# Optimization experiments

Measured on AMD Instinct MI355X. Metric: run time of the kernel, lower is better.

The kernel has to match this reference:

```python
import jax, jax.numpy as jnp
import numpy as np

N = 40000   # nodes
E = 500000  # edges
H = 2       # attention heads
C = 128     # d_graph_layer (in==out per layer)
L = 3       # n_graph_layer
G = 800     # graphs in batch
FIN = 56    # 2 * N_atom_features
NEG = 0.2   # leaky relu slope (PyG GATConv default)


def setup_inputs() -> dict:
    key = jax.random.key(0)
    ks = jax.random.split(key, 20)
    f32 = jnp.float32
    x = jax.random.normal(ks[0], (N, FIN), f32)
    edge_index = jax.random.randint(ks[1], (2, E), 0, N, jnp.int32)
    edge_attr = jax.random.uniform(ks[2], (E, 2), f32)
    valid = (jax.random.uniform(ks[3], (N, 2)) > 0.5).astype(f32)
    batch_idx = jnp.sort(jax.random.randint(ks[4], (N,), 0, G, jnp.int32))
    s = lambda k, shp, fan: jax.random.normal(k, shp, f32) / np.sqrt(fan).astype(np.float32)
    W_emb = s(ks[5], (FIN, C), FIN)
    Wg = s(ks[6], (L, C, H * C), C)           # per-layer GAT linear
    att_src = s(ks[7], (L, H, C), C)
    att_dst = s(ks[8], (L, H, C), C)
    We = s(ks[9], (L, 1, H * C), 1)           # edge_dim=1 projection
    att_e = s(ks[10], (L, H, C), C)
    bg = jnp.zeros((L, C), f32)
    gw = s(ks[11], (L, 2 * C, 1), 2 * C)      # gate linear
    gb = jnp.zeros((L, 1), f32)
    fc_w0 = s(ks[12], (2 * C, 128), 2 * C); fc_b0 = jnp.zeros((128,), f32)
    fc_w1 = s(ks[13], (128, 128), 128); fc_b1 = jnp.zeros((128,), f32)
    fc_w2 = s(ks[14], (128, 128), 128); fc_b2 = jnp.zeros((128,), f32)
    fc_w3 = s(ks[15], (128, 2), 128); fc_b3 = jnp.zeros((2,), f32)
    mu = jnp.array(0.5, f32)
    dev = jnp.array(1.0, f32)
    return dict(x=x, edge_index=edge_index, edge_attr=edge_attr, valid=valid,
                batch_idx=batch_idx, mu=mu, dev=dev, W_emb=W_emb, Wg=Wg,
                att_src=att_src, att_dst=att_dst, We=We, att_e=att_e, bg=bg,
                gw=gw, gb=gb, fc_w0=fc_w0, fc_b0=fc_b0, fc_w1=fc_w1, fc_b1=fc_b1,
                fc_w2=fc_w2, fc_b2=fc_b2, fc_w3=fc_w3, fc_b3=fc_b3)


def _seg_softmax(logits, seg, n):
    # softmax over incoming edges grouped by destination node
    m = jax.ops.segment_max(logits, seg, num_segments=n)
    e = jnp.exp(logits - m[seg])
    s = jax.ops.segment_sum(e, seg, num_segments=n)
    return e / (s[seg] + 1e-16)


def _gat_gate(h, src, dst, ea, Wk, a_s, a_d, Wek, a_e, bk, gwk, gbk):
    # edge-conditioned multi-head GAT with gated residual (concat=False -> head mean)
    n = h.shape[0]
    hh = (h @ Wk).reshape(n, H, C)                      # [N,H,C]
    ls = (hh * a_s[None]).sum(-1)                        # [N,H]
    ld = (hh * a_d[None]).sum(-1)
    eh = (ea @ Wek).reshape(-1, H, C)                    # [E,H,C]
    le = (eh * a_e[None]).sum(-1)                        # [E,H]
    logit = jax.nn.leaky_relu(ls[src] + ld[dst] + le, NEG)
    alpha = _seg_softmax(logit, dst, n)                  # [E,H]
    out = jax.ops.segment_sum(alpha[:, :, None] * hh[src], dst, num_segments=n)
    out = out.mean(1) + bk                               # head-average, [N,C]
    z = jax.nn.sigmoid(jnp.concatenate([h, out], -1) @ gwk + gbk)
    return z * h + (1.0 - z) * jax.nn.relu(out)


def reference(x, edge_index, edge_attr, valid, batch_idx, mu, dev, W_emb, Wg,
              att_src, att_dst, We, att_e, bg, gw, gb, fc_w0, fc_b0, fc_w1,
              fc_b1, fc_w2, fc_b2, fc_w3, fc_b3):
    src, dst = edge_index[0], edge_index[1]
    h = x @ W_emb
    a1 = edge_attr[:, 0:1]
    a2 = jnp.exp(-(edge_attr[:, 1:2] - mu) ** 2 / dev) + a1  # RBF + covalent
    for k in range(L):  # small fixed layer count
        h1 = _gat_gate(h, src, dst, a1, Wg[k], att_src[k], att_dst[k], We[k], att_e[k], bg[k], gw[k], gb[k])
        h2 = _gat_gate(h, src, dst, a2, Wg[k], att_src[k], att_dst[k], We[k], att_e[k], bg[k], gw[k], gb[k])
        h = h2 - h1
    gl = jax.ops.segment_sum(h * valid[:, 0:1], batch_idx, num_segments=G)
    gp = jax.ops.segment_sum(h * valid[:, 1:2], batch_idx, num_segments=G)
    o = jnp.concatenate([gl, gp], -1)                    # [G, 2C]
    o = jax.nn.relu(o @ fc_w0 + fc_b0)
    o = jax.nn.relu(o @ fc_w1 + fc_b1)
    o = jax.nn.relu(o @ fc_w2 + fc_b2)
    o = o @ fc_w3 + fc_b3
    return jnp.stack([o[:, 0], jnp.exp(o[:, 1])], axis=1)
```

## Files before the change

### kernel.cpp

```cpp
#include <hip/hip_runtime.h>
#include <hip/hip_fp16.h>
#include <math.h>

#define NN 40000
#define EE 500000
#define CC 128
#define GG 800
#define FINN 56
#define NEGS 0.2f
#define CAP 48

typedef _Float16 f16x8 __attribute__((ext_vector_type(8)));
typedef float f32x4 __attribute__((ext_vector_type(4)));

__device__ __forceinline__ float lrelu(float x) { return x > 0.f ? x : NEGS * x; }

#define WGSZ (3 * 256 * 128)
#define WESZ (128 * 64)
#define PREPN ((WGSZ + WESZ) / 256)

__global__ void k_prep(const float* __restrict__ Wg, const float* __restrict__ W_emb,
                       const float* __restrict__ We, const float* __restrict__ ate,
                       __half* __restrict__ Wt, __half* __restrict__ Wet,
                       float* __restrict__ wd, int* __restrict__ deg) {
    int gi = blockIdx.x * 256 + threadIdx.x;
    if (gi < NN) deg[gi] = 0;
    if (blockIdx.x == PREPN) {
        if (threadIdx.x < 64) {
            int lane = threadIdx.x;
            for (int idx = 0; idx < 6; ++idx) {
                const float* w = We + idx * 128;
                const float* a = ate + idx * 128;
                float p = w[lane] * a[lane] + w[lane + 64] * a[lane + 64];
                #pragma unroll
                for (int m = 32; m; m >>= 1) p += __shfl_xor(p, m);
                if (lane == 0) wd[idx] = p;
            }
        }
        return;
    }
    if (gi < WGSZ) {
        int l = gi >> 15, rem = gi & 32767;
        int c = rem >> 7, kk = rem & 127;
        Wt[gi] = __float2half_rn(Wg[l * 32768 + kk * 256 + c]);
    } else {
        int j = gi - WGSZ;
        int c = j >> 6, kk = j & 63;
        Wet[j] = (kk < FINN) ? __float2half_rn(W_emb[kk * CC + c]) : __half(0.f);
    }
}

__global__ void k_scatter(const int* __restrict__ ei, const float* __restrict__ ea,
                          const float* __restrict__ mu, const float* __restrict__ dev,
                          int* __restrict__ deg, int4* __restrict__ slab) {
    int e = blockIdx.x * 256 + threadIdx.x;
    if (e >= EE) return;
    int s = ei[e], d = ei[EE + e];
    float a1 = ea[2 * e];
    float xx = ea[2 * e + 1] - mu[0];
    float a2 = __expf(-xx * xx / dev[0]) + a1;
    int p = atomicAdd(&deg[d], 1);
    if (p < CAP) slab[d * CAP + p] = make_int4(s, __float_as_int(a1), __float_as_int(a2), 0);
}

__global__ __launch_bounds__(128) void k_embed16(
    const float* __restrict__ x, const __half* __restrict__ Wet,
    float* __restrict__ h, __half* __restrict__ h16) {
    __shared__ __half tile[16][136];
    int tid = threadIdx.x;
    int wave = tid >> 6, lane = tid & 63;
    int row0 = blockIdx.x * 16;
    int rlo = lane & 15, kgrp = lane >> 4;
    const float* xrow = x + (row0 + rlo) * FINN;
    f16x8 a0, a1;
    #pragma unroll
    for (int j = 0; j < 8; ++j) a0[j] = (_Float16)xrow[kgrp * 8 + j];
    #pragma unroll
    for (int j = 0; j < 8; ++j) {
        int k = 32 + kgrp * 8 + j;
        a1[j] = (k < FINN) ? (_Float16)xrow[k] : (_Float16)0.f;
    }
    #pragma unroll
    for (int nt = 0; nt < 4; ++nt) {
        int col = wave * 64 + nt * 16 + rlo;
        f32x4 acc = {0.f, 0.f, 0.f, 0.f};
        const __half* bbase = Wet + col * 64 + kgrp * 8;
        acc = __builtin_amdgcn_mfma_f32_16x16x32_f16(a0, *(const f16x8*)(bbase), acc, 0, 0, 0);
        acc = __builtin_amdgcn_mfma_f32_16x16x32_f16(a1, *(const f16x8*)(bbase + 32), acc, 0, 0, 0);
        #pragma unroll
        for (int r = 0; r < 4; ++r) {
            int row = row0 + kgrp * 4 + r;
            h[row * CC + col] = acc[r];
            tile[kgrp * 4 + r][col] = __float2half_rn(acc[r]);
        }
    }
    __syncthreads();
    int row = tid >> 3, chunk = tid & 7;
    uint4 a = *(uint4*)&tile[row][chunk * 16];
    uint4 b = *(uint4*)&tile[row][chunk * 16 + 8];
    __half* dst = &h16[(row0 + row) * CC + chunk * 16];
    *(uint4*)dst = a;
    *(uint4*)(dst + 8) = b;
}

__global__ __launch_bounds__(256) void k_gemm16(
    const __half* __restrict__ h16, const __half* __restrict__ Wt,
    const float* __restrict__ as_, const float* __restrict__ ad_,
    __half* __restrict__ hh16, float* __restrict__ lsld) {
    __shared__ __half tile[16][264];
    __shared__ float2 red[16][4];
    int tid = threadIdx.x;
    int wave = tid >> 6, lane = tid & 63;
    int row0 = blockIdx.x * 16;
    int rlo = lane & 15, kgrp = lane >> 4;
    f16x8 afrag[4];
    const __half* abase = h16 + (row0 + rlo) * CC + kgrp * 8;
    #pragma unroll
    for (int ks = 0; ks < 4; ++ks) afrag[ks] = *(const f16x8*)(abase + ks * 32);
    int head = wave >> 1;
    const float* as_h = as_ + head * CC;
    const float* ad_h = ad_ + head * CC;
    float psum[4] = {0.f, 0.f, 0.f, 0.f}, pdsum[4] = {0.f, 0.f, 0.f, 0.f};
    #pragma unroll
    for (int nt = 0; nt < 4; ++nt) {
        int col = wave * 64 + nt * 16 + rlo;
        f32x4 acc = {0.f, 0.f, 0.f, 0.f};
        const __half* bbase = Wt + col * CC + kgrp * 8;
        #pragma unroll
        for (int ks = 0; ks < 4; ++ks) {
            f16x8 bfrag = *(const f16x8*)(bbase + ks * 32);
            acc = __builtin_amdgcn_mfma_f32_16x16x32_f16(afrag[ks], bfrag, acc, 0, 0, 0);
        }
        float av = as_h[col & 127], dv = ad_h[col & 127];
        #pragma unroll
        for (int r = 0; r < 4; ++r) {
            float v = acc[r];
            tile[kgrp * 4 + r][col] = __float2half_rn(v);
            psum[r] += v * av;
            pdsum[r] += v * dv;
        }
    }
    #pragma unroll
    for (int r = 0; r < 4; ++r) {
        #pragma unroll
        for (int m = 1; m < 16; m <<= 1) {
            psum[r] += __shfl_xor(psum[r], m);
            pdsum[r] += __shfl_xor(pdsum[r], m);
        }
    }
    if (rlo == 0) {
        #pragma unroll
        for (int r = 0; r < 4; ++r) red[kgrp * 4 + r][wave] = make_float2(psum[r], pdsum[r]);
    }
    __syncthreads();
    {
        int row = tid >> 4, chunk = tid & 15;
        uint4 a = *(uint4*)&tile[row][chunk * 16];
        uint4 b = *(uint4*)&tile[row][chunk * 16 + 8];
        __half* dst = &hh16[(row0 + row) * 256 + chunk * 16];
        *(uint4*)dst = a;
        *(uint4*)(dst + 8) = b;
    }
    if (tid < 64) {
        int row = tid >> 2, which = tid & 3;
        float v;
        if (which == 0)      v = red[row][0].x + red[row][1].x;
        else if (which == 1) v = red[row][2].x + red[row][3].x;
        else if (which == 2) v = red[row][0].y + red[row][1].y;
        else                 v = red[row][2].y + red[row][3].y;
        lsld[(row0 + row) * 4 + which] = v;
    }
}

__global__ __launch_bounds__(256) void k_attn(
    const __half* __restrict__ hh16, const float* __restrict__ hcur,
    const float* __restrict__ lsld,
    const int* __restrict__ deg, const int4* __restrict__ slab,
    const float* __restrict__ wd, const float* __restrict__ bg,
    const float* __restrict__ gw, const float* __restrict__ gb,
    float* __restrict__ hout, __half* __restrict__ h16out) {
    __shared__ float4 evM[8][32];
    __shared__ int    evS[8][32];
    int tid = threadIdx.x;
    int sub = tid & 31;
    int hw = tid >> 5;
    int n = blockIdx.x * 8 + hw;
    float wd0 = wd[0], wd1 = wd[1];
    float4 nld = *(const float4*)&lsld[n * 4];
    float ld0 = nld.z, ld1 = nld.w;
    int count = min(deg[n], CAP);
    const int4* srow = slab + n * CAP;
    int hd01 = sub >> 4;
    float s0 = 0, s1 = 0, s2 = 0, s3 = 0;
    float acc1[8] = {0,0,0,0,0,0,0,0}, acc2[8] = {0,0,0,0,0,0,0,0};
    const char* hbase = (const char*)hh16 + sub * 16;

    for (int j0 = 0; j0 < count; j0 += 32) {
        int nact = min(32, count - j0);
        float4 e4 = make_float4(0.f, 0.f, 0.f, 0.f);
        int smine = 0;
        if (j0 + sub < count) {
            int4 c = srow[j0 + sub];
            smine = c.x;
            float a1 = __int_as_float(c.y), a2 = __int_as_float(c.z);
            float2 lsv = *(const float2*)&lsld[smine * 4];
            float b0 = lsv.x + ld0, b1 = lsv.y + ld1;
            e4.x = __expf(fminf(lrelu(b0 + a1 * wd0), 80.f));
            e4.y = __expf(fminf(lrelu(b0 + a2 * wd0), 80.f));
            e4.z = __expf(fminf(lrelu(b1 + a1 * wd1), 80.f));
            e4.w = __expf(fminf(lrelu(b1 + a2 * wd1), 80.f));
            s0 += e4.x; s1 += e4.y; s2 += e4.z; s3 += e4.w;
        }
        evM[hw][sub] = e4;
        evS[hw][sub] = smine * 512;
        int npv = (nact + 1) & ~1;
        for (int jj = 0; jj < npv; jj += 2) {
            float4 emA = evM[hw][jj], emB = evM[hw][jj + 1];
            int oA = evS[hw][jj], oB = evS[hw][jj + 1];
            union { uint4 u; _Float16 hx[8]; } rA, rB;
            rA.u = *(const uint4*)(hbase + oA);
            rB.u = *(const uint4*)(hbase + oB);
            float eA1 = hd01 ? emA.z : emA.x, eA2 = hd01 ? emA.w : emA.y;
            float eB1 = hd01 ? emB.z : emB.x, eB2 = hd01 ? emB.w : emB.y;
            #pragma unroll
            for (int i = 0; i < 8; ++i) {
                float vA = (float)rA.hx[i], vB = (float)rB.hx[i];
                acc1[i] += eA1 * vA; acc2[i] += eA2 * vA;
                acc1[i] += eB1 * vB; acc2[i] += eB2 * vB;
            }
        }
    }
    #pragma unroll
    for (int m = 16; m; m >>= 1) {
        s0 += __shfl_xor(s0, m); s1 += __shfl_xor(s1, m);
        s2 += __shfl_xor(s2, m); s3 += __shfl_xor(s3, m);
    }
    float d1 = (hd01 ? s2 : s0) + 1e-16f;
    float d2 = (hd01 ? s3 : s1) + 1e-16f;
    float id1 = 1.f / d1, id2 = 1.f / d2;
    int c0 = (sub & 15) * 8;
    float o1[8], o2[8];
    #pragma unroll
    for (int i = 0; i < 8; ++i) { o1[i] = acc1[i] * id1; o2[i] = acc2[i] * id2; }
    #pragma unroll
    for (int i = 0; i < 8; ++i) {
        o1[i] = 0.5f * (o1[i] + __shfl_xor(o1[i], 16)) + bg[c0 + i];
        o2[i] = 0.5f * (o2[i] + __shfl_xor(o2[i], 16)) + bg[c0 + i];
    }
    float hv[8];
    *(float4*)&hv[0] = ((const float4*)hcur)[n * 32 + (sub & 15) * 2];
    *(float4*)&hv[4] = ((const float4*)hcur)[n * 32 + (sub & 15) * 2 + 1];
    float pp1 = 0.f, pp2 = 0.f;
    if (sub < 16) {
        #pragma unroll
        for (int i = 0; i < 8; ++i) {
            pp1 += o1[i] * gw[128 + c0 + i];
            pp2 += o2[i] * gw[128 + c0 + i];
        }
    } else {
        float hp = 0.f;
        #pragma unroll
        for (int i = 0; i < 8; ++i) hp += hv[i] * gw[c0 + i];
        pp1 = hp; pp2 = hp;
    }
    #pragma unroll
    for (int m = 16; m; m >>= 1) { pp1 += __shfl_xor(pp1, m); pp2 += __shfl_xor(pp2, m); }
    float z1 = 1.f / (1.f + __expf(-(pp1 + gb[0])));
    float z2 = 1.f / (1.f + __expf(-(pp2 + gb[0])));
    if (sub < 16) {
        float r[8];
        #pragma unroll
        for (int i = 0; i < 8; ++i) {
            float g1 = z1 * hv[i] + (1.f - z1) * fmaxf(o1[i], 0.f);
            float g2 = z2 * hv[i] + (1.f - z2) * fmaxf(o2[i], 0.f);
            r[i] = g2 - g1;
        }
        ((float4*)hout)[n * 32 + (sub & 15) * 2]     = make_float4(r[0], r[1], r[2], r[3]);
        ((float4*)hout)[n * 32 + (sub & 15) * 2 + 1] = make_float4(r[4], r[5], r[6], r[7]);
        union { __half h[8]; uint4 u; } pk;
        #pragma unroll
        for (int i = 0; i < 8; ++i) pk.h[i] = __float2half_rn(r[i]);
        *(uint4*)&h16out[n * CC + c0] = pk.u;
    }
}

__global__ __launch_bounds__(128) void k_readmlp(
    const float* __restrict__ h, const float* __restrict__ valid, const int* __restrict__ batch,
    const float* __restrict__ w0, const float* __restrict__ b0,
    const float* __restrict__ w1, const float* __restrict__ b1,
    const float* __restrict__ w2, const float* __restrict__ b2,
    const float* __restrict__ w3, const float* __restrict__ b3,
    float* __restrict__ out) {
    __shared__ float cur[256];
    __shared__ float nxt[128];
    int g = blockIdx.x, t = threadIdx.x;
    int lo = 0, hi = NN;
    while (lo < hi) { int mid = (lo + hi) >> 1; if (batch[mid] < g) lo = mid + 1; else hi = mid; }
    int s = lo;
    lo = s; hi = NN;
    while (lo < hi) { int mid = (lo + hi) >> 1; if (batch[mid] < g + 1) lo = mid + 1; else hi = mid; }
    int e = lo;
    float gl = 0, gp = 0;
    for (int n = s; n < e; ++n) {
        float hv = h[n * CC + t];
        gl += hv * valid[2 * n];
        gp += hv * valid[2 * n + 1];
    }
    cur[t] = gl; cur[t + 128] = gp;
    __syncthreads();
    float ss = b0[t];
    for (int i = 0; i < 256; ++i) ss += cur[i] * w0[i * 128 + t];
    nxt[t] = fmaxf(ss, 0.f);
    __syncthreads();
    ss = b1[t];
    for (int i = 0; i < 128; ++i) ss += nxt[i] * w1[i * 128 + t];
    cur[t] = fmaxf(ss, 0.f);
    __syncthreads();
    ss = b2[t];
    for (int i = 0; i < 128; ++i) ss += cur[i] * w2[i * 128 + t];
    nxt[t] = fmaxf(ss, 0.f);
    __syncthreads();
    if (t < 2) {
        float o = b3[t];
        for (int i = 0; i < 128; ++i) o += nxt[i] * w3[i * 2 + t];
        out[g * 2 + t] = (t == 1) ? expf(o) : o;
    }
}

extern "C" void kernel_launch(void* const* d_in, const int* in_sizes, int n_in,
                              void* d_out, int out_size, void* d_ws, size_t ws_size,
                              hipStream_t stream) {
    const float* x      = (const float*)d_in[0];
    const int*   ei     = (const int*)d_in[1];
    const float* ea     = (const float*)d_in[2];
    const float* valid  = (const float*)d_in[3];
    const int*   batch  = (const int*)d_in[4];
    const float* mu     = (const float*)d_in[5];
    const float* devp   = (const float*)d_in[6];
    const float* W_emb  = (const float*)d_in[7];
    const float* Wg     = (const float*)d_in[8];
    const float* att_s  = (const float*)d_in[9];
    const float* att_d  = (const float*)d_in[10];
    const float* We     = (const float*)d_in[11];
    const float* att_e  = (const float*)d_in[12];
    const float* bg     = (const float*)d_in[13];
    const float* gw     = (const float*)d_in[14];
    const float* gb     = (const float*)d_in[15];
    const float* fw0    = (const float*)d_in[16];
    const float* fb0    = (const float*)d_in[17];
    const float* fw1    = (const float*)d_in[18];
    const float* fb1    = (const float*)d_in[19];
    const float* fw2    = (const float*)d_in[20];
    const float* fb2    = (const float*)d_in[21];
    const float* fw3    = (const float*)d_in[22];
    const float* fb3    = (const float*)d_in[23];
    float* out = (float*)d_out;

    char* p = (char*)d_ws;
    auto alloc = [&](size_t bytes) -> char* {
        char* r = p;
        p += (bytes + 255) & ~(size_t)255;
        return r;
    };
    float*  h0      = (float*)alloc((size_t)NN * CC * 4);
    float*  h1      = (float*)alloc((size_t)NN * CC * 4);
    __half* h16a    = (__half*)alloc((size_t)NN * CC * 2);
    __half* h16b    = (__half*)alloc((size_t)NN * CC * 2);
    __half* hh16    = (__half*)alloc((size_t)NN * 256 * 2);
    __half* Wt      = (__half*)alloc((size_t)3 * 256 * 128 * 2);
    __half* Wet     = (__half*)alloc((size_t)128 * 64 * 2);
    float*  lsld    = (float*)alloc((size_t)NN * 4 * 4);
    int*    deg     = (int*)alloc((size_t)NN * 4);
    int4*   slab    = (int4*)alloc((size_t)NN * CAP * 16);
    float*  wd      = (float*)alloc(256);

    k_prep<<<PREPN + 1, 256, 0, stream>>>(Wg, W_emb, We, att_e, Wt, Wet, wd, deg);
    k_scatter<<<(EE + 255) / 256, 256, 0, stream>>>(ei, ea, mu, devp, deg, slab);
    k_embed16<<<NN / 16, 128, 0, stream>>>(x, Wet, h0, h16a);

    float*  hc = h0;     float*  hn = h1;
    __half* hc16 = h16a; __half* hn16 = h16b;
    for (int k = 0; k < 3; ++k) {
        k_gemm16<<<NN / 16, 256, 0, stream>>>(hc16, Wt + (size_t)k * 32768,
                                              att_s + k * 256, att_d + k * 256, hh16, lsld);
        k_attn<<<NN / 8, 256, 0, stream>>>(hh16, hc, lsld, deg, slab,
                                           wd + k * 2, bg + k * 128, gw + k * 256, gb + k,
                                           hn, hn16);
        float* t1 = hc; hc = hn; hn = t1;
        __half* t2 = hc16; hc16 = hn16; hn16 = t2;
    }

    k_readmlp<<<GG, 128, 0, stream>>>(hc, valid, batch,
                                      fw0, fb0, fw1, fb1, fw2, fb2, fw3, fb3, out);
}
```

Measured before the change: 416.2 us.

## Aggregate low-dimension features before the GAT linear and fold attention into weights

Uses linearity to reorder each GAT layer. The attention kernel now gathers the 128-wide fp16 node features per edge and writes softmax-weighted sums for both heads and both edge variants. A new output GEMM then applies the per-head weight (pre-scaled by 0.5 for head averaging), the bias and the gated combination. The attention logit vectors and the gate's h-term are folded into precomputed weight vectors, so per-node logits are produced as epilogues of the embed and output kernels, which removes the separate per-layer GEMM kernel. This halves the bytes gathered per edge, at the cost of writing and reading a larger 512-wide aggregation buffer per node.

After: 469.8 us. +12.9%, slower.

```diff
diff --git a/kernel.cpp b/kernel.cpp
--- a/kernel.cpp
+++ b/kernel.cpp
@@ -15,38 +15,45 @@
 
 __device__ __forceinline__ float lrelu(float x) { return x > 0.f ? x : NEGS * x; }
 
-#define WGSZ (3 * 256 * 128)
-#define WESZ (128 * 64)
-#define PREPN ((WGSZ + WESZ) / 256)
+#define WT2SZ (3 * 128 * 256)
+#define WETSZ (128 * 64)
+#define VECSZ (3 * 256)
+#define PTOT  (WT2SZ + WETSZ + VECSZ + 6)
 
 __global__ void k_prep(const float* __restrict__ Wg, const float* __restrict__ W_emb,
+                       const float* __restrict__ as_, const float* __restrict__ ad_,
                        const float* __restrict__ We, const float* __restrict__ ate,
-                       __half* __restrict__ Wt, __half* __restrict__ Wet,
+                       __half* __restrict__ Wt2, __half* __restrict__ Wet,
+                       float* __restrict__ wsv, float* __restrict__ wdv,
                        float* __restrict__ wd, int* __restrict__ deg) {
     int gi = blockIdx.x * 256 + threadIdx.x;
     if (gi < NN) deg[gi] = 0;
-    if (blockIdx.x == PREPN) {
-        if (threadIdx.x < 64) {
-            int lane = threadIdx.x;
-            for (int idx = 0; idx < 6; ++idx) {
-                const float* w = We + idx * 128;
-                const float* a = ate + idx * 128;
-                float p = w[lane] * a[lane] + w[lane + 64] * a[lane + 64];
-                #pragma unroll
-                for (int m = 32; m; m >>= 1) p += __shfl_xor(p, m);
-                if (lane == 0) wd[idx] = p;
-            }
-        }
-        return;
-    }
-    if (gi < WGSZ) {
-        int l = gi >> 15, rem = gi & 32767;
-        int c = rem >> 7, kk = rem & 127;
-        Wt[gi] = __float2half_rn(Wg[l * 32768 + kk * 256 + c]);
-    } else {
-        int j = gi - WGSZ;
+    if (gi < WT2SZ) {
+        int k = gi >> 15, rem = gi & 32767;
+        int c = rem >> 8, kp = rem & 255;
+        int h = kp >> 7, K = kp & 127;
+        Wt2[gi] = __float2half_rn(0.5f * Wg[k * 32768 + K * 256 + h * 128 + c]);
+    } else if (gi < WT2SZ + WETSZ) {
+        int j = gi - WT2SZ;
         int c = j >> 6, kk = j & 63;
         Wet[j] = (kk < FINN) ? __float2half_rn(W_emb[kk * CC + c]) : __half(0.f);
+    } else if (gi < WT2SZ + WETSZ + VECSZ) {
+        int j = gi - WT2SZ - WETSZ;
+        int k = j >> 8, rem = j & 255;
+        int h = rem >> 7, K = rem & 127;
+        float ps = 0.f, pd = 0.f;
+        const float* wrow = Wg + k * 32768 + K * 256 + h * 128;
+        const float* arow = as_ + k * 256 + h * 128;
+        const float* drow = ad_ + k * 256 + h * 128;
+        for (int c = 0; c < 128; ++c) { float w = wrow[c]; ps += w * arow[c]; pd += w * drow[c]; }
+        wsv[j] = ps; wdv[j] = pd;
+    } else if (gi < PTOT) {
+        int idx = gi - WT2SZ - WETSZ - VECSZ;
+        const float* w = We + idx * 128;
+        const float* a = ate + idx * 128;
+        float p = 0.f;
+        for (int c = 0; c < 128; ++c) p += w[c] * a[c];
+        wd[idx] = p;
     }
 }
 
@@ -65,10 +72,10 @@
 
 __global__ __launch_bounds__(128) void k_embed16(
     const float* __restrict__ x, const __half* __restrict__ Wet,
-    float* __restrict__ h, __half* __restrict__ h16) {
+    const float* __restrict__ wsv0, const float* __restrict__ wdv0, const float* __restrict__ gw0,
+    float* __restrict__ h, __half* __restrict__ h16, float* __restrict__ lsld) {
     __shared__ __half tile[16][136];
-    int tid = threadIdx.x;
-    int wave = tid >> 6, lane = tid & 63;
+    int tid = threadIdx.x, wave = tid >> 6, lane = tid & 63;
     int row0 = blockIdx.x * 16;
     int rlo = lane & 15, kgrp = lane >> 4;
     const float* xrow = x + (row0 + rlo) * FINN;
@@ -95,105 +102,51 @@
         }
     }
     __syncthreads();
-    int row = tid >> 3, chunk = tid & 7;
-    uint4 a = *(uint4*)&tile[row][chunk * 16];
-    uint4 b = *(uint4*)&tile[row][chunk * 16 + 8];
-    __half* dst = &h16[(row0 + row) * CC + chunk * 16];
-    *(uint4*)dst = a;
-    *(uint4*)(dst + 8) = b;
-}
-
-__global__ __launch_bounds__(256) void k_gemm16(
-    const __half* __restrict__ h16, const __half* __restrict__ Wt,
-    const float* __restrict__ as_, const float* __restrict__ ad_,
-    __half* __restrict__ hh16, float* __restrict__ lsld) {
-    __shared__ __half tile[16][264];
-    __shared__ float2 red[16][4];
-    int tid = threadIdx.x;
-    int wave = tid >> 6, lane = tid & 63;
-    int row0 = blockIdx.x * 16;
-    int rlo = lane & 15, kgrp = lane >> 4;
-    f16x8 afrag[4];
-    const __half* abase = h16 + (row0 + rlo) * CC + kgrp * 8;
-    #pragma unroll
-    for (int ks = 0; ks < 4; ++ks) afrag[ks] = *(const f16x8*)(abase + ks * 32);
-    int head = wave >> 1;
-    const float* as_h = as_ + head * CC;
-    const float* ad_h = ad_ + head * CC;
-    float psum[4] = {0.f, 0.f, 0.f, 0.f}, pdsum[4] = {0.f, 0.f, 0.f, 0.f};
-    #pragma unroll
-    for (int nt = 0; nt < 4; ++nt) {
-        int col = wave * 64 + nt * 16 + rlo;
-        f32x4 acc = {0.f, 0.f, 0.f, 0.f};
-        const __half* bbase = Wt + col * CC + kgrp * 8;
-        #pragma unroll
-        for (int ks = 0; ks < 4; ++ks) {
-            f16x8 bfrag = *(const f16x8*)(bbase + ks * 32);
-            acc = __builtin_amdgcn_mfma_f32_16x16x32_f16(afrag[ks], bfrag, acc, 0, 0, 0);
-        }
-        float av = as_h[col & 127], dv = ad_h[col & 127];
-        #pragma unroll
-        for (int r = 0; r < 4; ++r) {
-            float v = acc[r];
-            tile[kgrp * 4 + r][col] = __float2half_rn(v);
-            psum[r] += v * av;
-            pdsum[r] += v * dv;
-        }
-    }
-    #pragma unroll
-    for (int r = 0; r < 4; ++r) {
-        #pragma unroll
-        for (int m = 1; m < 16; m <<= 1) {
-            psum[r] += __shfl_xor(psum[r], m);
-            pdsum[r] += __shfl_xor(pdsum[r], m);
-        }
-    }
-    if (rlo == 0) {
-        #pragma unroll
-        for (int r = 0; r < 4; ++r) red[kgrp * 4 + r][wave] = make_float2(psum[r], pdsum[r]);
-    }
-    __syncthreads();
     {
-        int row = tid >> 4, chunk = tid & 15;
+        int row = tid >> 3, chunk = tid & 7;
         uint4 a = *(uint4*)&tile[row][chunk * 16];
         uint4 b = *(uint4*)&tile[row][chunk * 16 + 8];
-        __half* dst = &hh16[(row0 + row) * 256 + chunk * 16];
+        __half* dst = &h16[(row0 + row) * CC + chunk * 16];
         *(uint4*)dst = a;
         *(uint4*)(dst + 8) = b;
     }
-    if (tid < 64) {
-        int row = tid >> 2, which = tid & 3;
-        float v;
-        if (which == 0)      v = red[row][0].x + red[row][1].x;
-        else if (which == 1) v = red[row][2].x + red[row][3].x;
-        else if (which == 2) v = red[row][0].y + red[row][1].y;
-        else                 v = red[row][2].y + red[row][3].y;
-        lsld[(row0 + row) * 4 + which] = v;
+    {
+        int row = tid >> 3, t8 = tid & 7, cb = t8 * 16;
+        float p0 = 0, p1 = 0, p2 = 0, p3 = 0, p4 = 0;
+        #pragma unroll
+        for (int c = 0; c < 16; ++c) {
+            float v = (float)tile[row][cb + c];
+            p0 += v * wsv0[cb + c];       p1 += v * wsv0[128 + cb + c];
+            p2 += v * wdv0[cb + c];       p3 += v * wdv0[128 + cb + c];
+            p4 += v * gw0[cb + c];
+        }
+        #pragma unroll
+        for (int m = 1; m < 8; m <<= 1) {
+            p0 += __shfl_xor(p0, m); p1 += __shfl_xor(p1, m); p2 += __shfl_xor(p2, m);
+            p3 += __shfl_xor(p3, m); p4 += __shfl_xor(p4, m);
+        }
+        if (t8 == 0) {
+            float* L = &lsld[(row0 + row) * 8];
+            L[0] = p0; L[1] = p1; L[2] = p2; L[3] = p3; L[4] = p4;
+        }
     }
 }
 
 __global__ __launch_bounds__(256) void k_attn(
-    const __half* __restrict__ hh16, const float* __restrict__ hcur,
-    const float* __restrict__ lsld,
+    const __half* __restrict__ h16, const float* __restrict__ lsld,
     const int* __restrict__ deg, const int4* __restrict__ slab,
-    const float* __restrict__ wd, const float* __restrict__ bg,
-    const float* __restrict__ gw, const float* __restrict__ gb,
-    float* __restrict__ hout, __half* __restrict__ h16out) {
+    const float* __restrict__ wd, __half* __restrict__ agg) {
     __shared__ float4 evM[8][32];
     __shared__ int    evS[8][32];
-    int tid = threadIdx.x;
-    int sub = tid & 31;
-    int hw = tid >> 5;
+    int tid = threadIdx.x, sub = tid & 31, hw = tid >> 5;
     int n = blockIdx.x * 8 + hw;
     float wd0 = wd[0], wd1 = wd[1];
-    float4 nld = *(const float4*)&lsld[n * 4];
-    float ld0 = nld.z, ld1 = nld.w;
+    float ld0 = lsld[n * 8 + 2], ld1 = lsld[n * 8 + 3];
     int count = min(deg[n], CAP);
     const int4* srow = slab + n * CAP;
-    int hd01 = sub >> 4;
     float s0 = 0, s1 = 0, s2 = 0, s3 = 0;
-    float acc1[8] = {0,0,0,0,0,0,0,0}, acc2[8] = {0,0,0,0,0,0,0,0};
-    const char* hbase = (const char*)hh16 + sub * 16;
+    float acc0[4] = {0,0,0,0}, acc1[4] = {0,0,0,0}, acc2[4] = {0,0,0,0}, acc3[4] = {0,0,0,0};
+    const char* hbase = (const char*)h16 + sub * 8;
 
     for (int j0 = 0; j0 < count; j0 += 32) {
         int nact = min(32, count - j0);
@@ -203,7 +156,7 @@
             int4 c = srow[j0 + sub];
             smine = c.x;
             float a1 = __int_as_float(c.y), a2 = __int_as_float(c.z);
-            float2 lsv = *(const float2*)&lsld[smine * 4];
+            float2 lsv = *(const float2*)&lsld[smine * 8];
             float b0 = lsv.x + ld0, b1 = lsv.y + ld1;
             e4.x = __expf(fminf(lrelu(b0 + a1 * wd0), 80.f));
             e4.y = __expf(fminf(lrelu(b0 + a2 * wd0), 80.f));
@@ -212,21 +165,21 @@
             s0 += e4.x; s1 += e4.y; s2 += e4.z; s3 += e4.w;
         }
         evM[hw][sub] = e4;
-        evS[hw][sub] = smine * 512;
+        evS[hw][sub] = smine * 256;
         int npv = (nact + 1) & ~1;
         for (int jj = 0; jj < npv; jj += 2) {
             float4 emA = evM[hw][jj], emB = evM[hw][jj + 1];
             int oA = evS[hw][jj], oB = evS[hw][jj + 1];
-            union { uint4 u; _Float16 hx[8]; } rA, rB;
-            rA.u = *(const uint4*)(hbase + oA);
-            rB.u = *(const uint4*)(hbase + oB);
-            float eA1 = hd01 ? emA.z : emA.x, eA2 = hd01 ? emA.w : emA.y;
-            float eB1 = hd01 ? emB.z : emB.x, eB2 = hd01 ? emB.w : emB.y;
+            union { uint2 u; _Float16 hx[4]; } rA, rB;
+            rA.u = *(const uint2*)(hbase + oA);
+            rB.u = *(const uint2*)(hbase + oB);
             #pragma unroll
-            for (int i = 0; i < 8; ++i) {
+            for (int i = 0; i < 4; ++i) {
                 float vA = (float)rA.hx[i], vB = (float)rB.hx[i];
-                acc1[i] += eA1 * vA; acc2[i] += eA2 * vA;
-                acc1[i] += eB1 * vB; acc2[i] += eB2 * vB;
+                acc0[i] += emA.x * vA + emB.x * vB;
+                acc1[i] += emA.y * vA + emB.y * vB;
+                acc2[i] += emA.z * vA + emB.z * vB;
+                acc3[i] += emA.w * vA + emB.w * vB;
             }
         }
     }
@@ -235,52 +188,114 @@
         s0 += __shfl_xor(s0, m); s1 += __shfl_xor(s1, m);
         s2 += __shfl_xor(s2, m); s3 += __shfl_xor(s3, m);
     }
-    float d1 = (hd01 ? s2 : s0) + 1e-16f;
-    float d2 = (hd01 ? s3 : s1) + 1e-16f;
-    float id1 = 1.f / d1, id2 = 1.f / d2;
-    int c0 = (sub & 15) * 8;
-    float o1[8], o2[8];
-    #pragma unroll
-    for (int i = 0; i < 8; ++i) { o1[i] = acc1[i] * id1; o2[i] = acc2[i] * id2; }
-    #pragma unroll
-    for (int i = 0; i < 8; ++i) {
-        o1[i] = 0.5f * (o1[i] + __shfl_xor(o1[i], 16)) + bg[c0 + i];
-        o2[i] = 0.5f * (o2[i] + __shfl_xor(o2[i], 16)) + bg[c0 + i];
-    }
-    float hv[8];
-    *(float4*)&hv[0] = ((const float4*)hcur)[n * 32 + (sub & 15) * 2];
-    *(float4*)&hv[4] = ((const float4*)hcur)[n * 32 + (sub & 15) * 2 + 1];
-    float pp1 = 0.f, pp2 = 0.f;
-    if (sub < 16) {
-        #pragma unroll
-        for (int i = 0; i < 8; ++i) {
-            pp1 += o1[i] * gw[128 + c0 + i];
-            pp2 += o2[i] * gw[128 + c0 + i];
-        }
-    } else {
-        float hp = 0.f;
-        #pragma unroll
-        for (int i = 0; i < 8; ++i) hp += hv[i] * gw[c0 + i];
-        pp1 = hp; pp2 = hp;
-    }
-    #pragma unroll
-    for (int m = 16; m; m >>= 1) { pp1 += __shfl_xor(pp1, m); pp2 += __shfl_xor(pp2, m); }
-    float z1 = 1.f / (1.f + __expf(-(pp1 + gb[0])));
-    float z2 = 1.f / (1.f + __expf(-(pp2 + gb[0])));
-    if (sub < 16) {
-        float r[8];
-        #pragma unroll
-        for (int i = 0; i < 8; ++i) {
-            float g1 = z1 * hv[i] + (1.f - z1) * fmaxf(o1[i], 0.f);
-            float g2 = z2 * hv[i] + (1.f - z2) * fmaxf(o2[i], 0.f);
-            r[i] = g2 - g1;
-        }
-        ((float4*)hout)[n * 32 + (sub & 15) * 2]     = make_float4(r[0], r[1], r[2], r[3]);
-        ((float4*)hout)[n * 32 + (sub & 15) * 2 + 1] = make_float4(r[4], r[5], r[6], r[7]);
-        union { __half h[8]; uint4 u; } pk;
-        #pragma unroll
-        for (int i = 0; i < 8; ++i) pk.h[i] = __float2half_rn(r[i]);
-        *(uint4*)&h16out[n * CC + c0] = pk.u;
+    float i0 = 1.f / (s0 + 1e-16f), i1 = 1.f / (s1 + 1e-16f);
+    float i2 = 1.f / (s2 + 1e-16f), i3 = 1.f / (s3 + 1e-16f);
+    union { __half h[4]; uint2 u; } pk;
+    __half* base = agg + (size_t)n * 512;
+    #pragma unroll
+    for (int i = 0; i < 4; ++i) pk.h[i] = __float2half_rn(acc0[i] * i0);
+    *(uint2*)&base[sub * 4] = pk.u;
+    #pragma unroll
+    for (int i = 0; i < 4; ++i) pk.h[i] = __float2half_rn(acc2[i] * i2);
+    *(uint2*)&base[128 + sub * 4] = pk.u;
+    #pragma unroll
+    for (int i = 0; i < 4; ++i) pk.h[i] = __float2half_rn(acc1[i] * i1);
+    *(uint2*)&base[256 + sub * 4] = pk.u;
+    #pragma unroll
+    for (int i = 0; i < 4; ++i) pk.h[i] = __float2half_rn(acc3[i] * i3);
+    *(uint2*)&base[384 + sub * 4] = pk.u;
+}
+
+__global__ __launch_bounds__(256) void k_outgemm(
+    const __half* __restrict__ agg, const __half* __restrict__ Wt2k,
+    const float* __restrict__ bgk, const float* __restrict__ gwk, const float* __restrict__ gbk,
+    const float* __restrict__ hcur, const float* __restrict__ lsld,
+    const float* __restrict__ wsvn, const float* __restrict__ wdvn, const float* __restrict__ gwn,
+    float* __restrict__ hout, __half* __restrict__ h16out, float* __restrict__ lsldout) {
+    __shared__ float red[16][4];
+    __shared__ float zbuf[16];
+    __shared__ __half tile[8][136];
+    int tid = threadIdx.x, wave = tid >> 6, lane = tid & 63;
+    int row0 = blockIdx.x * 16, nb0 = blockIdx.x * 8;
+    int rlo = lane & 15, kgrp = lane >> 4;
+    f16x8 af[8];
+    const __half* ab = agg + (size_t)(row0 + rlo) * 256 + kgrp * 8;
+    #pragma unroll
+    for (int ks = 0; ks < 8; ++ks) af[ks] = *(const f16x8*)(ab + ks * 32);
+    float of[2][4];
+    float pout[4] = {0, 0, 0, 0};
+    #pragma unroll
+    for (int nt = 0; nt < 2; ++nt) {
+        int col = wave * 32 + nt * 16 + rlo;
+        f32x4 acc = {0.f, 0.f, 0.f, 0.f};
+        const __half* bb = Wt2k + col * 256 + kgrp * 8;
+        #pragma unroll
+        for (int ks = 0; ks < 8; ++ks)
+            acc = __builtin_amdgcn_mfma_f32_16x16x32_f16(af[ks], *(const f16x8*)(bb + ks * 32), acc, 0, 0, 0);
+        float bgv = bgk[col], gv = gwk[128 + col];
+        #pragma unroll
+        for (int r = 0; r < 4; ++r) {
+            float o = acc[r] + bgv;
+            of[nt][r] = o;
+            pout[r] += o * gv;
+        }
+    }
+    #pragma unroll
+    for (int r = 0; r < 4; ++r) {
+        #pragma unroll
+        for (int m = 1; m < 16; m <<= 1) pout[r] += __shfl_xor(pout[r], m);
+    }
+    if (rlo == 0) {
+        #pragma unroll
+        for (int r = 0; r < 4; ++r) red[kgrp * 4 + r][wave] = pout[r];
+    }
+    __syncthreads();
+    if (tid < 16) {
+        float pr = red[tid][0] + red[tid][1] + red[tid][2] + red[tid][3];
+        int node = (row0 + tid) >> 1;
+        zbuf[tid] = 1.f / (1.f + __expf(-(pr + lsld[node * 8 + 4] + gbk[0])));
+    }
+    __syncthreads();
+    #pragma unroll
+    for (int nt = 0; nt < 2; ++nt) {
+        int col = wave * 32 + nt * 16 + rlo;
+        #pragma unroll
+        for (int p = 0; p < 2; ++p) {
+            int rowe = kgrp * 4 + 2 * p;
+            int node = nb0 + kgrp * 2 + p;
+            float o1 = of[nt][2 * p], o2 = of[nt][2 * p + 1];
+            float z1 = zbuf[rowe], z2 = zbuf[rowe + 1];
+            float hv = hcur[node * CC + col];
+            float val = (z2 - z1) * hv + (1.f - z2) * fmaxf(o2, 0.f) - (1.f - z1) * fmaxf(o1, 0.f);
+            hout[node * CC + col] = val;
+            tile[kgrp * 2 + p][col] = __float2half_rn(val);
+        }
+    }
+    __syncthreads();
+    {
+        int node = tid >> 5, off = (tid & 31) * 4;
+        uint2 v = *(uint2*)&tile[node][off];
+        *(uint2*)&h16out[(nb0 + node) * CC + off] = v;
+    }
+    {
+        int node = tid >> 5, sub = tid & 31, cb = sub * 4;
+        float p0 = 0, p1 = 0, p2 = 0, p3 = 0, p4 = 0;
+        #pragma unroll
+        for (int c = 0; c < 4; ++c) {
+            float v = (float)tile[node][cb + c];
+            p0 += v * wsvn[cb + c];       p1 += v * wsvn[128 + cb + c];
+            p2 += v * wdvn[cb + c];       p3 += v * wdvn[128 + cb + c];
+            p4 += v * gwn[cb + c];
+        }
+        #pragma unroll
+        for (int m = 1; m < 32; m <<= 1) {
+            p0 += __shfl_xor(p0, m); p1 += __shfl_xor(p1, m); p2 += __shfl_xor(p2, m);
+            p3 += __shfl_xor(p3, m); p4 += __shfl_xor(p4, m);
+        }
+        if (sub == 0) {
+            float* L = &lsldout[(nb0 + node) * 8];
+            L[0] = p0; L[1] = p1; L[2] = p2; L[3] = p3; L[4] = p4;
+        }
     }
 }
 
@@ -366,26 +381,31 @@
     float*  h1      = (float*)alloc((size_t)NN * CC * 4);
     __half* h16a    = (__half*)alloc((size_t)NN * CC * 2);
     __half* h16b    = (__half*)alloc((size_t)NN * CC * 2);
-    __half* hh16    = (__half*)alloc((size_t)NN * 256 * 2);
-    __half* Wt      = (__half*)alloc((size_t)3 * 256 * 128 * 2);
-    __half* Wet     = (__half*)alloc((size_t)128 * 64 * 2);
-    float*  lsld    = (float*)alloc((size_t)NN * 4 * 4);
+    __half* aggbuf  = (__half*)alloc((size_t)NN * 512 * 2);
+    __half* Wt2     = (__half*)alloc((size_t)WT2SZ * 2);
+    __half* Wet     = (__half*)alloc((size_t)WETSZ * 2);
+    float*  wsv     = (float*)alloc((size_t)VECSZ * 4);
+    float*  wdv     = (float*)alloc((size_t)VECSZ * 4);
+    float*  lsld    = (float*)alloc((size_t)NN * 8 * 4);
     int*    deg     = (int*)alloc((size_t)NN * 4);
     int4*   slab    = (int4*)alloc((size_t)NN * CAP * 16);
     float*  wd      = (float*)alloc(256);
 
-    k_prep<<<PREPN + 1, 256, 0, stream>>>(Wg, W_emb, We, att_e, Wt, Wet, wd, deg);
+    k_prep<<<(PTOT + 255) / 256, 256, 0, stream>>>(Wg, W_emb, att_s, att_d, We, att_e,
+                                                   Wt2, Wet, wsv, wdv, wd, deg);
     k_scatter<<<(EE + 255) / 256, 256, 0, stream>>>(ei, ea, mu, devp, deg, slab);
-    k_embed16<<<NN / 16, 128, 0, stream>>>(x, Wet, h0, h16a);
+    k_embed16<<<NN / 16, 128, 0, stream>>>(x, Wet, wsv, wdv, gw, h0, h16a, lsld);
 
     float*  hc = h0;     float*  hn = h1;
     __half* hc16 = h16a; __half* hn16 = h16b;
     for (int k = 0; k < 3; ++k) {
-        k_gemm16<<<NN / 16, 256, 0, stream>>>(hc16, Wt + (size_t)k * 32768,
-                                              att_s + k * 256, att_d + k * 256, hh16, lsld);
-        k_attn<<<NN / 8, 256, 0, stream>>>(hh16, hc, lsld, deg, slab,
-                                           wd + k * 2, bg + k * 128, gw + k * 256, gb + k,
-                                           hn, hn16);
+        int kn = (k < 2) ? k + 1 : 2;
+        k_attn<<<NN / 8, 256, 0, stream>>>(hc16, lsld, deg, slab, wd + k * 2, aggbuf);
+        k_outgemm<<<NN / 8, 256, 0, stream>>>(aggbuf, Wt2 + (size_t)k * 32768,
+                                              bg + k * 128, gw + k * 256, gb + k,
+                                              hc, lsld,
+                                              wsv + kn * 256, wdv + kn * 256, gw + kn * 256,
+                                              hn, hn16, lsld);
         float* t1 = hc; hc = hn; hn = t1;
         __half* t2 = hc16; hc16 = hn16; hn16 = t2;
     }
```
